# Performance work log

Hardware: AMD Instinct MI355X
Metric: run time of the kernel (lower is better)

The kernel has to match this reference:

```python
import jax, jax.numpy as jnp
import numpy as np

S = 4096   # decoder sequence length
T = 4096   # encoder sequence length
D = 2048   # x_size == qk_size (required for q @ k^T to typecheck)


def setup_inputs() -> dict:
    key = jax.random.key(0)
    k1, k2, k3, k4 = jax.random.split(key, 4)
    x_vectors = jax.random.normal(k1, (S, D), dtype=jnp.float32)
    enc_output = jax.random.normal(k2, (2, T, S), dtype=jnp.float32) * 0.02
    Wq = jax.random.normal(k3, (D, D), dtype=jnp.float32) * 0.02
    bq = jax.random.normal(k4, (D,), dtype=jnp.float32) * 0.02
    return {"x_vectors": x_vectors, "enc_output": enc_output, "Wq": Wq, "bq": bq}


def reference(x_vectors, enc_output, Wq, bq):
    # q = Linear(x): [S, D]
    q = x_vectors @ Wq.T + bq
    # k, v produced by matmul of encoder-output matrices with x: [T, D]
    k = enc_output[0] @ x_vectors
    v = enc_output[1] @ x_vectors
    # attention scores [S, T], scaled by sqrt(qk_size)
    e = (q @ k.T) / jnp.sqrt(jnp.float32(D))
    # softmax over dim=1 (last axis of the rank-2 score matrix)
    a = jax.nn.softmax(e, axis=1)
    # z = a @ v^T: [S, D]
    z = a @ v
    return z
```

## Files before the change

kernel.cpp:

```cpp
#include <hip/hip_runtime.h>


typedef __attribute__((ext_vector_type(8))) __bf16 bf16x8;
typedef __attribute__((ext_vector_type(4))) float f32x4;
typedef __attribute__((ext_vector_type(4))) unsigned short ushort4v;
typedef __attribute__((ext_vector_type(8))) unsigned short ushort8v;

#define S_DIM 4096
#define T_DIM 4096
#define D_DIM 2048

__device__ __forceinline__ unsigned short f2bf(float f) {
    unsigned int u = __float_as_uint(f);
    u += 0x7fffu + ((u >> 16) & 1u);
    return (unsigned short)(u >> 16);
}

__device__ __forceinline__ void block_sync() {
    __builtin_amdgcn_sched_barrier(0);
    __builtin_amdgcn_s_barrier();
    __builtin_amdgcn_sched_barrier(0);
}

#define GL(gptr, sptr)                                                        \
    __builtin_amdgcn_global_load_lds(                                         \
        (__attribute__((address_space(1))) void*)(void*)(gptr),               \
        (__attribute__((address_space(3))) void*)(sptr), 16, 0, 0)

__device__ __forceinline__ f32x4 MFMA16(bf16x8 a, bf16x8 b, f32x4 c) {
    return __builtin_amdgcn_mfma_f32_16x16x32_bf16(a, b, c, 0, 0, 0);
}

__global__ __launch_bounds__(256)
void k_convert(const float* __restrict__ in, unsigned short* __restrict__ out, long n) {
    long i = ((long)blockIdx.x * blockDim.x + threadIdx.x) * 8;
    const long stride = (long)gridDim.x * blockDim.x * 8;
    for (; i < n; i += stride) {
        float4 a = *(const float4*)(in + i);
        float4 b = *(const float4*)(in + i + 4);
        ushort8v o;
        o[0] = f2bf(a.x); o[1] = f2bf(a.y); o[2] = f2bf(a.z); o[3] = f2bf(a.w);
        o[4] = f2bf(b.x); o[5] = f2bf(b.y); o[6] = f2bf(b.z); o[7] = f2bf(b.w);
        *(ushort8v*)(out + i) = o;
    }
}

__global__ __launch_bounds__(256)
void k_transpose_dual(const float* __restrict__ in,
                      unsigned short* __restrict__ outT,
                      unsigned short* __restrict__ outN, int R, int C) {
    __shared__ float tile[32][33];
    const int bx = blockIdx.x * 32;
    const int by = blockIdx.y * 32;
    const int tx = threadIdx.x;
    const int ty = threadIdx.y;
    #pragma unroll
    for (int i = 0; i < 32; i += 8) {
        float v = in[(long)(by + ty + i) * C + bx + tx];
        tile[ty + i][tx] = v;
        outN[(long)(by + ty + i) * C + bx + tx] = f2bf(v);
    }
    __syncthreads();
    #pragma unroll
    for (int i = 0; i < 32; i += 8)
        outT[(long)(bx + ty + i) * R + by + tx] = f2bf(tile[tx][ty + i]);
}

__global__ __launch_bounds__(256)
void k_transpose_bf(const unsigned short* __restrict__ in,
                    unsigned short* __restrict__ out, int R, int C) {
    __shared__ unsigned short tile[32][33];
    const int bx = blockIdx.x * 32;
    const int by = blockIdx.y * 32;
    const int tx = threadIdx.x;
    const int ty = threadIdx.y;
    #pragma unroll
    for (int i = 0; i < 32; i += 8)
        tile[ty + i][tx] = in[(long)(by + ty + i) * C + bx + tx];
    __syncthreads();
    #pragma unroll
    for (int i = 0; i < 32; i += 8)
        out[(long)(bx + ty + i) * R + by + tx] = tile[tx][ty + i];
}

template<bool STG, bool PF, int VMW>
__device__ __forceinline__ void seg8(
    const unsigned short* (&gA)[2], const int (&ldA)[2],
    const unsigned short* (&gB)[2], const int (&ldB)[2],
    const char* cur, const char* nxt, char* stg, int arB, int brB,
    bf16x8 (&Ac)[8], bf16x8 (&B01c)[2], bf16x8 (&B23)[2],
    bf16x8 (&An)[8], bf16x8 (&B01n)[2],
    f32x4 (&acc)[8][4])
{
    B23[0] = *(const bf16x8*)(cur + brB + 2048);
    B23[1] = *(const bf16x8*)(cur + brB + 3072);
    if constexpr (STG) {
        GL(gA[0], stg + ldA[0]); gA[0] += 32;
        GL(gA[1], stg + ldA[1]); gA[1] += 32;
    }
    block_sync();
    asm volatile("s_waitcnt lgkmcnt(2)" ::: "memory");
    __builtin_amdgcn_sched_barrier(0);
    __builtin_amdgcn_s_setprio(1);
    #pragma unroll
    for (int m = 0; m < 8; ++m) {
        acc[m][0] = MFMA16(Ac[m], B01c[0], acc[m][0]);
        acc[m][1] = MFMA16(Ac[m], B01c[1], acc[m][1]);
    }
    __builtin_amdgcn_s_setprio(0);
    if constexpr (PF) {
        #pragma unroll
        for (int m = 0; m < 8; ++m)
            An[m] = *(const bf16x8*)(nxt + arB + m * 1024);
        B01n[0] = *(const bf16x8*)(nxt + brB);
        B01n[1] = *(const bf16x8*)(nxt + brB + 1024);
    }
    if constexpr (STG) {
        GL(gB[0], stg + ldB[0]); gB[0] += 32;
        GL(gB[1], stg + ldB[1]); gB[1] += 32;
    }
    if constexpr (VMW == 4)      asm volatile("s_waitcnt vmcnt(4)" ::: "memory");
    else if constexpr (VMW == 0) asm volatile("s_waitcnt vmcnt(0)" ::: "memory");
    block_sync();
    if constexpr (PF) asm volatile("s_waitcnt lgkmcnt(10)" ::: "memory");
    else              asm volatile("s_waitcnt lgkmcnt(0)" ::: "memory");
    __builtin_amdgcn_sched_barrier(0);
    __builtin_amdgcn_s_setprio(1);
    #pragma unroll
    for (int m = 0; m < 8; ++m) {
        acc[m][2] = MFMA16(Ac[m], B23[0], acc[m][2]);
        acc[m][3] = MFMA16(Ac[m], B23[1], acc[m][3]);
    }
    __builtin_amdgcn_s_setprio(0);
}

template<bool STG, bool PF, int VMW>
__device__ __forceinline__ void seg4(
    const unsigned short* (&gA)[2], const int (&ldA)[2],
    const unsigned short* (&gB)[2], const int (&ldB)[2],
    const char* cur, const char* nxt, char* stg, int arB, int brB,
    bf16x8 (&Ac)[4], bf16x8 (&B01c)[2], bf16x8 (&B23)[2],
    bf16x8 (&An)[4], bf16x8 (&B01n)[2],
    f32x4 (&acc)[4][4])
{
    B23[0] = *(const bf16x8*)(cur + brB + 2048);
    B23[1] = *(const bf16x8*)(cur + brB + 3072);
    if constexpr (STG) {
        GL(gA[0], stg + ldA[0]); gA[0] += 32;
    }
    block_sync();
    asm volatile("s_waitcnt lgkmcnt(2)" ::: "memory");
    __builtin_amdgcn_sched_barrier(0);
    __builtin_amdgcn_s_setprio(1);
    #pragma unroll
    for (int m = 0; m < 4; ++m) {
        acc[m][0] = MFMA16(Ac[m], B01c[0], acc[m][0]);
        acc[m][1] = MFMA16(Ac[m], B01c[1], acc[m][1]);
    }
    __builtin_amdgcn_s_setprio(0);
    if constexpr (PF) {
        #pragma unroll
        for (int m = 0; m < 4; ++m)
            An[m] = *(const bf16x8*)(nxt + arB + m * 1024);
        B01n[0] = *(const bf16x8*)(nxt + brB);
        B01n[1] = *(const bf16x8*)(nxt + brB + 1024);
    }
    if constexpr (STG) {
        GL(gB[0], stg + ldB[0]); gB[0] += 32;
        GL(gB[1], stg + ldB[1]); gB[1] += 32;
    }
    if constexpr (VMW == 3)      asm volatile("s_waitcnt vmcnt(3)" ::: "memory");
    else if constexpr (VMW == 0) asm volatile("s_waitcnt vmcnt(0)" ::: "memory");
    block_sync();
    if constexpr (PF) asm volatile("s_waitcnt lgkmcnt(6)" ::: "memory");
    else              asm volatile("s_waitcnt lgkmcnt(0)" ::: "memory");
    __builtin_amdgcn_sched_barrier(0);
    __builtin_amdgcn_s_setprio(1);
    #pragma unroll
    for (int m = 0; m < 4; ++m) {
        acc[m][2] = MFMA16(Ac[m], B23[0], acc[m][2]);
        acc[m][3] = MFMA16(Ac[m], B23[1], acc[m][3]);
    }
    __builtin_amdgcn_s_setprio(0);
}

template<int MFR, int OUT_BF16, int HAS_BIAS>
__global__ __launch_bounds__(512, 2)
void k_gemm(const unsigned short* __restrict__ A,
            const unsigned short* __restrict__ B,
            const float* __restrict__ bias,
            void* __restrict__ C,
            int M, int N, int K, float alpha) {
    constexpr int BM   = MFR * 32;
    constexpr int LPTA = (BM * 4) / 512;
    constexpr int LDSA = BM * 64;
    constexpr int SLOT = LDSA + 16384;
    extern __shared__ __align__(16) char smem[];

    const int tid = threadIdx.x;
    const int l = tid & 63;
    const int w = tid >> 6;
    const int wr = w >> 2;
    const int wc = w & 3;

    const int gx = gridDim.x, gy = gridDim.y;
    const int flat = blockIdx.y * gx + blockIdx.x;
    const int per = (gx * gy) >> 3;
    const int wid = (flat & 7) * per + (flat >> 3);
    const int sc = wid / (gy * 4);
    const int rm = wid - sc * gy * 4;
    const int by = rm >> 2;
    const int bx = sc * 4 + (rm & 3);

    const long brow = (long)by * BM;
    const long bcol = (long)bx * 256;
    const int NT = K >> 5;

    const unsigned short* gA[2];
    int ldA[2];
    #pragma unroll
    for (int j = 0; j < LPTA; ++j) {
        const int q = (w * LPTA + j) * 64 + l;
        const int R = q >> 2;
        const int c = (q & 3) ^ ((R >> 1) & 3);
        gA[j] = A + (brow + R) * (long)K + c * 8;
        ldA[j] = q * 16;
    }
    const unsigned short* gB[2];
    int ldB[2];
    #pragma unroll
    for (int j = 0; j < 2; ++j) {
        const int q = (w * 2 + j) * 64 + l;
        const int R = q >> 2;
        const int c = (q & 3) ^ ((R >> 1) & 3);
        gB[j] = B + (bcol + R) * (long)K + c * 8;
        ldB[j] = LDSA + q * 16;
    }

    const int sAB = (((l >> 4) ^ ((l >> 1) & 3)) << 4);
    const int arB = (wr * (MFR * 16) + (l & 15)) * 64 + sAB;
    const int brB = LDSA + (wc * 64 + (l & 15)) * 64 + sAB;

    char* const b0 = smem;
    char* const b1 = smem + SLOT;
    char* const b2 = smem + 2 * SLOT;
    char* const b3 = smem + 3 * SLOT;

    {
        char* d = smem;
        #pragma unroll
        for (int tt = 0; tt < 3; ++tt) {
            #pragma unroll
            for (int j = 0; j < LPTA; ++j) { GL(gA[j], d + ldA[j]); gA[j] += 32; }
            #pragma unroll
            for (int j = 0; j < 2; ++j)    { GL(gB[j], d + ldB[j]); gB[j] += 32; }
            d += SLOT;
        }
        if constexpr (MFR == 8) asm volatile("s_waitcnt vmcnt(4)" ::: "memory");
        else                    asm volatile("s_waitcnt vmcnt(3)" ::: "memory");
        block_sync();
    }

    if constexpr (MFR == 8) {
        bf16x8 Aa[8], Ab[8], Ba[2], Bb[2], B23[2];
        #pragma unroll
        for (int m = 0; m < 8; ++m) Aa[m] = *(const bf16x8*)(b0 + arB + m * 1024);
        Ba[0] = *(const bf16x8*)(b0 + brB);
        Ba[1] = *(const bf16x8*)(b0 + brB + 1024);

        f32x4 acc[8][4] = {};
        for (int t = 0; t + 8 <= NT; t += 4) {
            seg8<true, true, 4>(gA, ldA, gB, ldB, b0, b1, b3, arB, brB,
                                Aa, Ba, B23, Ab, Bb, acc);
            seg8<true, true, 4>(gA, ldA, gB, ldB, b1, b2, b0, arB, brB,
                                Ab, Bb, B23, Aa, Ba, acc);
            seg8<true, true, 4>(gA, ldA, gB, ldB, b2, b3, b1, arB, brB,
                                Aa, Ba, B23, Ab, Bb, acc);
            seg8<true, true, 4>(gA, ldA, gB, ldB, b3, b0, b2, arB, brB,
                                Ab, Bb, B23, Aa, Ba, acc);
        }
        seg8<true,  true,  4>(gA, ldA, gB, ldB, b0, b1, b3, arB, brB,
                              Aa, Ba, B23, Ab, Bb, acc);
        seg8<false, true,  0>(gA, ldA, gB, ldB, b1, b2, b3, arB, brB,
                              Ab, Bb, B23, Aa, Ba, acc);
        seg8<false, true, -1>(gA, ldA, gB, ldB, b2, b3, b3, arB, brB,
                              Aa, Ba, B23, Ab, Bb, acc);
        seg8<false, false, -1>(gA, ldA, gB, ldB, b3, b0, b3, arB, brB,
                               Ab, Bb, B23, Aa, Ba, acc);

        const long crow0 = brow + wr * 128 + (l >> 4) * 4;
        const long ccol0 = bcol + wc * 64 + (l & 15);
        #pragma unroll
        for (int n = 0; n < 4; ++n) {
            const long col = ccol0 + n * 16;
            const float bb = HAS_BIAS ? bias[col] : 0.0f;
            #pragma unroll
            for (int m = 0; m < 8; ++m) {
                #pragma unroll
                for (int r = 0; r < 4; ++r) {
                    const long row = crow0 + m * 16 + r;
                    const float v = acc[m][n][r] * alpha + bb;
                    if (OUT_BF16)
                        ((unsigned short*)C)[row * N + col] = f2bf(v);
                    else
                        ((float*)C)[row * N + col] = v;
                }
            }
        }
    } else {
        bf16x8 Aa[4], Ab[4], Ba[2], Bb[2], B23[2];
        #pragma unroll
        for (int m = 0; m < 4; ++m) Aa[m] = *(const bf16x8*)(b0 + arB + m * 1024);
        Ba[0] = *(const bf16x8*)(b0 + brB);
        Ba[1] = *(const bf16x8*)(b0 + brB + 1024);

        f32x4 acc[4][4] = {};
        for (int t = 0; t + 8 <= NT; t += 4) {
            seg4<true, true, 3>(gA, ldA, gB, ldB, b0, b1, b3, arB, brB,
                                Aa, Ba, B23, Ab, Bb, acc);
            seg4<true, true, 3>(gA, ldA, gB, ldB, b1, b2, b0, arB, brB,
                                Ab, Bb, B23, Aa, Ba, acc);
            seg4<true, true, 3>(gA, ldA, gB, ldB, b2, b3, b1, arB, brB,
                                Aa, Ba, B23, Ab, Bb, acc);
            seg4<true, true, 3>(gA, ldA, gB, ldB, b3, b0, b2, arB, brB,
                                Ab, Bb, B23, Aa, Ba, acc);
        }
        seg4<true,  true,  3>(gA, ldA, gB, ldB, b0, b1, b3, arB, brB,
                              Aa, Ba, B23, Ab, Bb, acc);
        seg4<false, true,  0>(gA, ldA, gB, ldB, b1, b2, b3, arB, brB,
                              Ab, Bb, B23, Aa, Ba, acc);
        seg4<false, true, -1>(gA, ldA, gB, ldB, b2, b3, b3, arB, brB,
                              Aa, Ba, B23, Ab, Bb, acc);
        seg4<false, false, -1>(gA, ldA, gB, ldB, b3, b0, b3, arB, brB,
                               Ab, Bb, B23, Aa, Ba, acc);

        const long crow0 = brow + wr * 64 + (l >> 4) * 4;
        const long ccol0 = bcol + wc * 64 + (l & 15);
        #pragma unroll
        for (int n = 0; n < 4; ++n) {
            const long col = ccol0 + n * 16;
            const float bb = HAS_BIAS ? bias[col] : 0.0f;
            #pragma unroll
            for (int m = 0; m < 4; ++m) {
                #pragma unroll
                for (int r = 0; r < 4; ++r) {
                    const long row = crow0 + m * 16 + r;
                    const float v = acc[m][n][r] * alpha + bb;
                    if (OUT_BF16)
                        ((unsigned short*)C)[row * N + col] = f2bf(v);
                    else
                        ((float*)C)[row * N + col] = v;
                }
            }
        }
    }
}

__global__ __launch_bounds__(256)
void k_softmax_bf(const unsigned short* __restrict__ E,
                  unsigned short* __restrict__ A, int T) {
    const long row = blockIdx.x;
    const unsigned short* er = E + row * (long)T;
    const int t = threadIdx.x;
    const int l = t & 63;
    const int w = t >> 6;

    float v[16];
    float m = -3.4e38f;
    #pragma unroll
    for (int j = 0; j < 2; ++j) {
        ushort8v u = *(const ushort8v*)(er + j * 2048 + t * 8);
        #pragma unroll
        for (int i = 0; i < 8; ++i) {
            v[j * 8 + i] = __uint_as_float((unsigned int)u[i] << 16);
            m = fmaxf(m, v[j * 8 + i]);
        }
    }
    #pragma unroll
    for (int o = 32; o > 0; o >>= 1) m = fmaxf(m, __shfl_xor(m, o));

    __shared__ float redm[4];
    __shared__ float reds[4];
    if (l == 0) redm[w] = m;
    __syncthreads();
    m = fmaxf(fmaxf(redm[0], redm[1]), fmaxf(redm[2], redm[3]));

    float s = 0.f;
    #pragma unroll
    for (int i = 0; i < 16; ++i) {
        v[i] = __expf(v[i] - m);
        s += v[i];
    }
    #pragma unroll
    for (int o = 32; o > 0; o >>= 1) s += __shfl_xor(s, o);
    if (l == 0) reds[w] = s;
    __syncthreads();
    s = reds[0] + reds[1] + reds[2] + reds[3];
    const float inv = 1.0f / s;

    unsigned short* ar = A + row * (long)T;
    #pragma unroll
    for (int j = 0; j < 2; ++j) {
        ushort8v o8;
        #pragma unroll
        for (int i = 0; i < 8; ++i) o8[i] = f2bf(v[j * 8 + i] * inv);
        *(ushort8v*)(ar + j * 2048 + t * 8) = o8;
    }
}

extern "C" void kernel_launch(void* const* d_in, const int* in_sizes, int n_in,
                              void* d_out, int out_size, void* d_ws, size_t ws_size,
                              hipStream_t stream) {
    const float* x   = (const float*)d_in[0];
    const float* enc = (const float*)d_in[1];
    const float* Wq  = (const float*)d_in[2];
    const float* bq  = (const float*)d_in[3];
    float* out = (float*)d_out;
    char* ws = (char*)d_ws;

    unsigned short* abf   = (unsigned short*)(ws);
    unsigned short* xT    = (unsigned short*)(ws);
    unsigned short* xbf   = (unsigned short*)(ws + (16L << 20));
    unsigned short* wqbf  = (unsigned short*)(ws + (32L << 20));
    unsigned short* qbf   = (unsigned short*)(ws + (40L << 20));
    unsigned short* kv    = (unsigned short*)(ws + (56L << 20));
    unsigned short* vT    = (unsigned short*)(ws + (88L << 20));
    unsigned short* encbf = (unsigned short*)(ws + (104L << 20));
    unsigned short* ebf   = (unsigned short*)(ws + (104L << 20));

    k_convert<<<4096, 256, 0, stream>>>(Wq,  wqbf,  (long)D_DIM * D_DIM);
    k_convert<<<4096, 256, 0, stream>>>(enc, encbf, 2L * T_DIM * S_DIM);
    k_transpose_dual<<<dim3(D_DIM / 32, S_DIM / 32), dim3(32, 8), 0, stream>>>(
        x, xT, xbf, S_DIM, D_DIM);

    #define LAUNCH_G(MFRV, OB, HB, Ap, Bp, biasp, Cp, M_, N_, K_, al)                      \
        do {                                                                               \
            constexpr int smemB = (MFRV * 32 * 64 + 16384) * 4;                            \
            hipFuncSetAttribute((const void*)k_gemm<MFRV, OB, HB>,                         \
                                hipFuncAttributeMaxDynamicSharedMemorySize, smemB);        \
            k_gemm<MFRV, OB, HB><<<dim3((N_) / 256, (M_) / (MFRV * 32)), 512, smemB,       \
                                   stream>>>(Ap, Bp, biasp, Cp, M_, N_, K_, al);           \
        } while (0)

    LAUNCH_G(4, 1, 1, xbf, wqbf, bq, qbf, S_DIM, D_DIM, D_DIM, 1.0f);
    LAUNCH_G(8, 1, 0, encbf, xT, nullptr, kv, 2 * T_DIM, D_DIM, S_DIM, 1.0f);
    k_transpose_bf<<<dim3(D_DIM / 32, T_DIM / 32), dim3(32, 8), 0, stream>>>(
        kv + (long)T_DIM * D_DIM, vT, T_DIM, D_DIM);
    LAUNCH_G(8, 1, 0, qbf, kv, nullptr, ebf, S_DIM, T_DIM, D_DIM, 0.022097086912079608f);
    k_softmax_bf<<<S_DIM, 256, 0, stream>>>(ebf, abf, T_DIM);
    LAUNCH_G(4, 0, 0, abf, vT, nullptr, out, S_DIM, D_DIM, T_DIM, 1.0f);
}
```

Before: 360.9 us.

## Interleave global and LDS loads with MFMAs and use a single barrier per segment

Each pipeline segment now does one barrier at its start. Global-to-LDS staging loads and next-tile LDS fragment reads are interleaved between small groups of MFMAs instead of being issued in separate blocks around two barriers. The vmcnt waits in the prologue and tail are loosened so the pipeline can run one tile deeper. The aim is to hide memory latency under matrix math and cut barrier stalls, at the risk of LDS hazards if the buffer reuse distance or waitcnt values are wrong.

```diff
diff --git a/kernel.cpp b/kernel.cpp
--- a/kernel.cpp
+++ b/kernel.cpp
@@ -3,7 +3,6 @@
 
 typedef __attribute__((ext_vector_type(8))) __bf16 bf16x8;
 typedef __attribute__((ext_vector_type(4))) float f32x4;
-typedef __attribute__((ext_vector_type(4))) unsigned short ushort4v;
 typedef __attribute__((ext_vector_type(8))) unsigned short ushort8v;
 
 #define S_DIM 4096
@@ -92,40 +91,57 @@
     bf16x8 (&An)[8], bf16x8 (&B01n)[2],
     f32x4 (&acc)[8][4])
 {
-    B23[0] = *(const bf16x8*)(cur + brB + 2048);
-    B23[1] = *(const bf16x8*)(cur + brB + 3072);
-    if constexpr (STG) {
-        GL(gA[0], stg + ldA[0]); gA[0] += 32;
-        GL(gA[1], stg + ldA[1]); gA[1] += 32;
-    }
-    block_sync();
-    asm volatile("s_waitcnt lgkmcnt(2)" ::: "memory");
-    __builtin_amdgcn_sched_barrier(0);
-    __builtin_amdgcn_s_setprio(1);
-    #pragma unroll
-    for (int m = 0; m < 8; ++m) {
-        acc[m][0] = MFMA16(Ac[m], B01c[0], acc[m][0]);
-        acc[m][1] = MFMA16(Ac[m], B01c[1], acc[m][1]);
-    }
-    __builtin_amdgcn_s_setprio(0);
-    if constexpr (PF) {
-        #pragma unroll
-        for (int m = 0; m < 8; ++m)
-            An[m] = *(const bf16x8*)(nxt + arB + m * 1024);
-        B01n[0] = *(const bf16x8*)(nxt + brB);
-        B01n[1] = *(const bf16x8*)(nxt + brB + 1024);
-    }
-    if constexpr (STG) {
-        GL(gB[0], stg + ldB[0]); gB[0] += 32;
-        GL(gB[1], stg + ldB[1]); gB[1] += 32;
-    }
     if constexpr (VMW == 4)      asm volatile("s_waitcnt vmcnt(4)" ::: "memory");
     else if constexpr (VMW == 0) asm volatile("s_waitcnt vmcnt(0)" ::: "memory");
     block_sync();
+    asm volatile("s_waitcnt lgkmcnt(0)" ::: "memory");
+    __builtin_amdgcn_sched_barrier(0);
+
+    B23[0] = *(const bf16x8*)(cur + brB + 2048);
+    B23[1] = *(const bf16x8*)(cur + brB + 3072);
+
+    __builtin_amdgcn_s_setprio(1);
+    acc[0][0] = MFMA16(Ac[0], B01c[0], acc[0][0]);
+    acc[0][1] = MFMA16(Ac[0], B01c[1], acc[0][1]);
+    acc[1][0] = MFMA16(Ac[1], B01c[0], acc[1][0]);
+    acc[1][1] = MFMA16(Ac[1], B01c[1], acc[1][1]);
+    if constexpr (STG) { GL(gA[0], stg + ldA[0]); gA[0] += 32; }
+    if constexpr (PF) {
+        An[0] = *(const bf16x8*)(nxt + arB);
+        An[1] = *(const bf16x8*)(nxt + arB + 1024);
+    }
+    acc[2][0] = MFMA16(Ac[2], B01c[0], acc[2][0]);
+    acc[2][1] = MFMA16(Ac[2], B01c[1], acc[2][1]);
+    acc[3][0] = MFMA16(Ac[3], B01c[0], acc[3][0]);
+    acc[3][1] = MFMA16(Ac[3], B01c[1], acc[3][1]);
+    if constexpr (STG) { GL(gA[1], stg + ldA[1]); gA[1] += 32; }
+    if constexpr (PF) {
+        An[2] = *(const bf16x8*)(nxt + arB + 2048);
+        An[3] = *(const bf16x8*)(nxt + arB + 3072);
+    }
+    acc[4][0] = MFMA16(Ac[4], B01c[0], acc[4][0]);
+    acc[4][1] = MFMA16(Ac[4], B01c[1], acc[4][1]);
+    acc[5][0] = MFMA16(Ac[5], B01c[0], acc[5][0]);
+    acc[5][1] = MFMA16(Ac[5], B01c[1], acc[5][1]);
+    if constexpr (STG) { GL(gB[0], stg + ldB[0]); gB[0] += 32; }
+    if constexpr (PF) {
+        An[4] = *(const bf16x8*)(nxt + arB + 4096);
+        An[5] = *(const bf16x8*)(nxt + arB + 5120);
+    }
+    acc[6][0] = MFMA16(Ac[6], B01c[0], acc[6][0]);
+    acc[6][1] = MFMA16(Ac[6], B01c[1], acc[6][1]);
+    acc[7][0] = MFMA16(Ac[7], B01c[0], acc[7][0]);
+    acc[7][1] = MFMA16(Ac[7], B01c[1], acc[7][1]);
+    if constexpr (STG) { GL(gB[1], stg + ldB[1]); gB[1] += 32; }
+    if constexpr (PF) {
+        An[6] = *(const bf16x8*)(nxt + arB + 6144);
+        An[7] = *(const bf16x8*)(nxt + arB + 7168);
+        B01n[0] = *(const bf16x8*)(nxt + brB);
+        B01n[1] = *(const bf16x8*)(nxt + brB + 1024);
+    }
     if constexpr (PF) asm volatile("s_waitcnt lgkmcnt(10)" ::: "memory");
     else              asm volatile("s_waitcnt lgkmcnt(0)" ::: "memory");
     __builtin_amdgcn_sched_barrier(0);
-    __builtin_amdgcn_s_setprio(1);
     #pragma unroll
     for (int m = 0; m < 8; ++m) {
         acc[m][2] = MFMA16(Ac[m], B23[0], acc[m][2]);
@@ -143,39 +159,42 @@
     bf16x8 (&An)[4], bf16x8 (&B01n)[2],
     f32x4 (&acc)[4][4])
 {
+    if constexpr (VMW == 3)      asm volatile("s_waitcnt vmcnt(3)" ::: "memory");
+    else if constexpr (VMW == 0) asm volatile("s_waitcnt vmcnt(0)" ::: "memory");
+    block_sync();
+    asm volatile("s_waitcnt lgkmcnt(0)" ::: "memory");
+    __builtin_amdgcn_sched_barrier(0);
+
     B23[0] = *(const bf16x8*)(cur + brB + 2048);
     B23[1] = *(const bf16x8*)(cur + brB + 3072);
-    if constexpr (STG) {
-        GL(gA[0], stg + ldA[0]); gA[0] += 32;
-    }
-    block_sync();
-    asm volatile("s_waitcnt lgkmcnt(2)" ::: "memory");
-    __builtin_amdgcn_sched_barrier(0);
+
     __builtin_amdgcn_s_setprio(1);
-    #pragma unroll
-    for (int m = 0; m < 4; ++m) {
-        acc[m][0] = MFMA16(Ac[m], B01c[0], acc[m][0]);
-        acc[m][1] = MFMA16(Ac[m], B01c[1], acc[m][1]);
-    }
-    __builtin_amdgcn_s_setprio(0);
-    if constexpr (PF) {
-        #pragma unroll
-        for (int m = 0; m < 4; ++m)
-            An[m] = *(const bf16x8*)(nxt + arB + m * 1024);
-        B01n[0] = *(const bf16x8*)(nxt + brB);
-        B01n[1] = *(const bf16x8*)(nxt + brB + 1024);
-    }
+    acc[0][0] = MFMA16(Ac[0], B01c[0], acc[0][0]);
+    acc[0][1] = MFMA16(Ac[0], B01c[1], acc[0][1]);
+    acc[1][0] = MFMA16(Ac[1], B01c[0], acc[1][0]);
+    acc[1][1] = MFMA16(Ac[1], B01c[1], acc[1][1]);
+    if constexpr (STG) { GL(gA[0], stg + ldA[0]); gA[0] += 32; }
+    if constexpr (PF) {
+        An[0] = *(const bf16x8*)(nxt + arB);
+        An[1] = *(const bf16x8*)(nxt + arB + 1024);
+    }
+    acc[2][0] = MFMA16(Ac[2], B01c[0], acc[2][0]);
+    acc[2][1] = MFMA16(Ac[2], B01c[1], acc[2][1]);
+    acc[3][0] = MFMA16(Ac[3], B01c[0], acc[3][0]);
+    acc[3][1] = MFMA16(Ac[3], B01c[1], acc[3][1]);
     if constexpr (STG) {
         GL(gB[0], stg + ldB[0]); gB[0] += 32;
         GL(gB[1], stg + ldB[1]); gB[1] += 32;
     }
-    if constexpr (VMW == 3)      asm volatile("s_waitcnt vmcnt(3)" ::: "memory");
-    else if constexpr (VMW == 0) asm volatile("s_waitcnt vmcnt(0)" ::: "memory");
-    block_sync();
+    if constexpr (PF) {
+        An[2] = *(const bf16x8*)(nxt + arB + 2048);
+        An[3] = *(const bf16x8*)(nxt + arB + 3072);
+        B01n[0] = *(const bf16x8*)(nxt + brB);
+        B01n[1] = *(const bf16x8*)(nxt + brB + 1024);
+    }
     if constexpr (PF) asm volatile("s_waitcnt lgkmcnt(6)" ::: "memory");
     else              asm volatile("s_waitcnt lgkmcnt(0)" ::: "memory");
     __builtin_amdgcn_sched_barrier(0);
-    __builtin_amdgcn_s_setprio(1);
     #pragma unroll
     for (int m = 0; m < 4; ++m) {
         acc[m][2] = MFMA16(Ac[m], B23[0], acc[m][2]);
@@ -256,8 +275,8 @@
             for (int j = 0; j < 2; ++j)    { GL(gB[j], d + ldB[j]); gB[j] += 32; }
             d += SLOT;
         }
-        if constexpr (MFR == 8) asm volatile("s_waitcnt vmcnt(4)" ::: "memory");
-        else                    asm volatile("s_waitcnt vmcnt(3)" ::: "memory");
+        if constexpr (MFR == 8) asm volatile("s_waitcnt vmcnt(8)" ::: "memory");
+        else                    asm volatile("s_waitcnt vmcnt(6)" ::: "memory");
         block_sync();
     }
 
@@ -281,9 +300,9 @@
         }
         seg8<true,  true,  4>(gA, ldA, gB, ldB, b0, b1, b3, arB, brB,
                               Aa, Ba, B23, Ab, Bb, acc);
-        seg8<false, true,  0>(gA, ldA, gB, ldB, b1, b2, b3, arB, brB,
+        seg8<false, true,  4>(gA, ldA, gB, ldB, b1, b2, b3, arB, brB,
                               Ab, Bb, B23, Aa, Ba, acc);
-        seg8<false, true, -1>(gA, ldA, gB, ldB, b2, b3, b3, arB, brB,
+        seg8<false, true,  0>(gA, ldA, gB, ldB, b2, b3, b3, arB, brB,
                               Aa, Ba, B23, Ab, Bb, acc);
         seg8<false, false, -1>(gA, ldA, gB, ldB, b3, b0, b3, arB, brB,
                                Ab, Bb, B23, Aa, Ba, acc);
@@ -327,9 +346,9 @@
         }
         seg4<true,  true,  3>(gA, ldA, gB, ldB, b0, b1, b3, arB, brB,
                               Aa, Ba, B23, Ab, Bb, acc);
-        seg4<false, true,  0>(gA, ldA, gB, ldB, b1, b2, b3, arB, brB,
+        seg4<false, true,  3>(gA, ldA, gB, ldB, b1, b2, b3, arB, brB,
                               Ab, Bb, B23, Aa, Ba, acc);
-        seg4<false, true, -1>(gA, ldA, gB, ldB, b2, b3, b3, arB, brB,
+        seg4<false, true,  0>(gA, ldA, gB, ldB, b2, b3, b3, arB, brB,
                               Aa, Ba, B23, Ab, Bb, acc);
         seg4<false, false, -1>(gA, ldA, gB, ldB, b3, b0, b3, arB, brB,
                                Ab, Bb, B23, Aa, Ba, acc);
```

New measurement: 364.8 us. No clear change (+1.1%).
